# Performance work log

Measured on AMD Instinct MI355X. Metric: run time of the kernel, lower is better.

## Reference

```python
import jax, jax.numpy as jnp
import numpy as np


def setup_inputs() -> dict:
    key = jax.random.key(0)
    k1, k2, k3 = jax.random.split(key, 3)
    x = jax.random.normal(k1, (32, 256, 32, 32), dtype=jnp.float32)
    weight = jax.random.normal(k2, (256, 256, 3, 3), dtype=jnp.float32) * 0.05
    bias = jax.random.normal(k3, (256,), dtype=jnp.float32) * 0.01
    return {"x": x, "weight": weight, "bias": bias}


def _forward(x, weight, bias):
    B, cin, n, _ = x.shape
    cout, _, k, _ = weight.shape
    s = (k - 1) // 2
    nf = n // 2 + 1
    bins = n * nf

    # fft shift matrix: exp(-1j*2*pi*s*(i+j)/n), kept rfft columns
    idx = jnp.arange(n)
    shift = idx[None, :] + idx[:, None]                     # (n, n)
    shift_m = jnp.exp(-1j * 2 * jnp.pi * s * shift / n)[:, :nf]
    shift_m = shift_m.reshape(bins, 1, 1).astype(jnp.complex64)

    # xfft: (B, cin, n, nf) -> (bins, cin, B)
    xfft = jnp.fft.rfft2(x)
    xfft = jnp.transpose(xfft, (2, 3, 1, 0)).reshape(bins, cin, B)

    # Hfft: (cout, cin, n, nf) -> (bins, cout, cin), shifted + conj
    Hfft = jnp.fft.rfft2(weight, s=(n, n)).reshape(cout, cin, bins)
    Hfft = shift_m * jnp.conj(jnp.transpose(Hfft, (2, 0, 1)))

    def sq_abs(z):
        return jnp.real(z) ** 2 + jnp.imag(z) ** 2

    RowNorm = jnp.sqrt(jnp.sum(sq_abs(Hfft), axis=2))       # (bins, cout)
    ColNorm = jnp.sqrt(jnp.sum(sq_abs(Hfft), axis=1))       # (bins, cin)

    if cout >= cin:
        RowLoss = jnp.mean((RowNorm - jnp.sqrt(cin / cout)) ** 2)
        ColLoss = jnp.mean((ColNorm - 1.0) ** 2)
        HHT = jnp.einsum('npc,nqc->npq', jnp.conj(Hfft), Hfft)  # (bins, cout, cout)
        mask = jnp.triu(jnp.ones((cout, cout), bool), k=1)
        count = bins * (cout * (cout - 1) // 2)
        AngLoss = jnp.sum(sq_abs(HHT) * mask[None]) / count   # MSE(|HHT[triu]|, 0)
        L = cout * ColLoss + cin * RowLoss + AngLoss
    else:
        RowLoss = jnp.mean((RowNorm - 1.0) ** 2)
        ColLoss = jnp.mean((ColNorm - jnp.sqrt(cout / cin)) ** 2)
        HTH = jnp.einsum('ndp,ndq->npq', jnp.conj(Hfft), Hfft)  # (bins, cin, cin)
        mask = jnp.triu(jnp.ones((cin, cin), bool), k=1)
        count = bins * (cin * (cin - 1) // 2)
        AngLoss = jnp.sum(sq_abs(HTH) * mask[None]) / count
        L = cout * ColLoss + cin * RowLoss + AngLoss

    # per-bin complex matmul: (bins, cout, cin) @ (bins, cin, B) -> (bins, cout, B)
    yfft = Hfft @ xfft
    yfft = jnp.transpose(yfft.reshape(n, nf, cout, B), (3, 2, 0, 1))  # (B, cout, n, nf)
    y = jnp.fft.irfft2(yfft, s=(n, n))
    y = y + bias[None, :, None, None]
    return y, L


def reference(x, weight, bias):
    return _forward(x, weight, bias)
```

## Files before the change

kernel.cpp:

```cpp
#include <hip/hip_runtime.h>
#include <math.h>

typedef __attribute__((ext_vector_type(8)))  short  short8;
typedef __attribute__((ext_vector_type(16))) float  float16;

#define TWO_PI_OVER_32 0.19634954084936207f

static __device__ __forceinline__ unsigned short f2bf(float f) {
    unsigned int u = __float_as_uint(f);
    u = (u + 0x7FFFu + ((u >> 16) & 1u)) >> 16;
    return (unsigned short)u;
}
static __device__ __forceinline__ float bf2f(unsigned short s) {
    return __uint_as_float(((unsigned int)s) << 16);
}

static __device__ __forceinline__ void g2l16(const void* g, void* l) {
    __builtin_amdgcn_global_load_lds(
        (const __attribute__((address_space(1))) unsigned int*)g,
        (__attribute__((address_space(3))) unsigned int*)l, 16, 0, 0);
}

#define SBAR() do { __builtin_amdgcn_s_barrier(); \
                    __builtin_amdgcn_sched_barrier(0); } while (0)
#define WAITV(n) do { asm volatile("s_waitcnt vmcnt(" #n ")" ::: "memory"); \
                      __builtin_amdgcn_sched_barrier(0); } while (0)

__global__ __launch_bounds__(256) void k_prepx(const float* __restrict__ x,
                                               unsigned short* __restrict__ xb,
                                               const float* __restrict__ w,
                                               unsigned short* __restrict__ wt,
                                               unsigned short* __restrict__ Vb,
                                               float* __restrict__ Drow,
                                               float* __restrict__ Dcol) {
    __shared__ union {
        unsigned short tr[8 * 1024];
        struct { float sdata[45]; float ws2[256 * 9]; } wm;
    } sh;
    int tid = threadIdx.x;

    if (blockIdx.x < 1024) {
        int b = blockIdx.x >> 5, cig = blockIdx.x & 31;
        int r = tid >> 3, c4 = (tid & 7) * 4;
        const float4* xv = (const float4*)(x + ((size_t)(b * 256 + cig * 8)) * 1024);
        #pragma unroll
        for (int u = 0; u < 8; ++u) {
            float4 v = xv[u * 256 + r * 8 + (c4 >> 2)];
            union { unsigned short s[4]; uint2 d; } pk;
            pk.s[0] = f2bf(v.x); pk.s[1] = f2bf(v.y);
            pk.s[2] = f2bf(v.z); pk.s[3] = f2bf(v.w);
            *(uint2*)&sh.tr[u * 1024 + r * 32 + c4] = pk.d;
        }
        __syncthreads();
        uint4* dst = (uint4*)xb + ((size_t)b * 32 + cig) * 1024;
        #pragma unroll
        for (int k = 0; k < 4; ++k) {
            int g = tid * 4 + k;
            union { unsigned short u[8]; uint4 v; } pk;
            #pragma unroll
            for (int u = 0; u < 8; ++u) pk.u[u] = sh.tr[u * 1024 + g];
            dst[g] = pk.v;
        }
        return;
    }

    int blk = blockIdx.x - 1024, lane = tid & 63;
    bool colmode = blk >= 256;
    int pc = blk & 255;
    if (tid < 45) sh.wm.sdata[tid] = 0.f;

    int p = colmode ? tid : pc;
    int c = colmode ? pc : tid;
    float w9[9];
    #pragma unroll
    for (int t = 0; t < 9; ++t) w9[t] = w[(p * 256 + c) * 9 + t];
    if (!colmode) {
        #pragma unroll
        for (int t = 0; t < 9; ++t) sh.wm.ws2[tid * 9 + t] = w9[t];
    }
    __syncthreads();

    int idx = 0;
    for (int ta = 0; ta < 9; ++ta)
        for (int tb = ta; tb < 9; ++tb) {
            float v = w9[ta] * w9[tb];
            #pragma unroll
            for (int off = 32; off > 0; off >>= 1) v += __shfl_down(v, off);
            if (lane == 0) atomicAdd(&sh.wm.sdata[idx], v);
            ++idx;
        }
    __syncthreads();
    if (tid < 45) (colmode ? Dcol : Drow)[tid * 256 + pc] = sh.wm.sdata[tid];

    if (!colmode) {
        #pragma unroll
        for (int t = 0; t < 9; ++t)
            wt[t * 65536 + (c >> 3) * 2048 + p * 8 + (c & 7)] = f2bf(w9[t]);
        if (tid < 320) {
            int ta = tid >> 5, cig = tid & 31;
            union { unsigned short u[8]; uint4 v; } pk;
            #pragma unroll
            for (int u = 0; u < 8; ++u)
                pk.u[u] = (ta < 9) ? f2bf(sh.wm.ws2[(cig * 8 + u) * 9 + ta]) : (unsigned short)0;
            ((uint4*)Vb)[(p * 10 + ta) * 32 + cig] = pk.v;
        }
    }
}

__global__ __launch_bounds__(256, 3) void k_conv(const unsigned short* __restrict__ xb,
                                                 const unsigned short* __restrict__ wt,
                                                 const float* __restrict__ bias,
                                                 const unsigned short* __restrict__ Vb,
                                                 unsigned short* __restrict__ Gb,
                                                 float* __restrict__ y) {
    __shared__ unsigned short xs[640 * 8];
    __shared__ unsigned short wsm[2][1152 * 8];

    const int tid  = threadIdx.x;
    const int lane = tid & 63;
    const int half = lane >> 5;
    const int m    = lane & 31;

    if (blockIdx.x < 210) {
        int blk = blockIdx.x, I = 0;
        while (blk >= 20 - I) { blk -= 20 - I; ++I; }
        int J = I + blk;
        const int wave = tid >> 6;
        const int wm = wave >> 1, wn = wave & 1;
        const int row0 = I * 128 + wm * 64;
        const int col0 = J * 128 + wn * 64;

        float16 acc[2][2];
        #pragma unroll
        for (int i = 0; i < 2; ++i)
            #pragma unroll
            for (int j = 0; j < 2; ++j)
                #pragma unroll
                for (int r = 0; r < 16; ++r) acc[i][j][r] = 0.f;

        const short8* vb = (const short8*)Vb;
        for (int kc = 0; kc < 16; ++kc) {
            int cig = kc * 2 + half;
            short8 a0 = vb[(row0 + m) * 32 + cig];
            short8 a1 = vb[(row0 + 32 + m) * 32 + cig];
            short8 b0 = vb[(col0 + m) * 32 + cig];
            short8 b1 = vb[(col0 + 32 + m) * 32 + cig];
            acc[0][0] = __builtin_amdgcn_mfma_f32_32x32x16_bf16(a0, b0, acc[0][0], 0, 0, 0);
            acc[0][1] = __builtin_amdgcn_mfma_f32_32x32x16_bf16(a0, b1, acc[0][1], 0, 0, 0);
            acc[1][0] = __builtin_amdgcn_mfma_f32_32x32x16_bf16(a1, b0, acc[1][0], 0, 0, 0);
            acc[1][1] = __builtin_amdgcn_mfma_f32_32x32x16_bf16(a1, b1, acc[1][1], 0, 0, 0);
        }
        #pragma unroll
        for (int i = 0; i < 2; ++i)
            #pragma unroll
            for (int j = 0; j < 2; ++j)
                #pragma unroll
                for (int reg = 0; reg < 16; ++reg) {
                    int crow = (reg & 3) + 8 * (reg >> 2) + 4 * half;
                    Gb[(row0 + i * 32 + crow) * 2560 + col0 + j * 32 + m] =
                        f2bf(acc[i][j][reg]);
                }
        return;
    }

    const int wv    = tid >> 6;
    const int id    = blockIdx.x - 210;
    const int xcd   = id & 7;
    const int local = id >> 3;
    const int b     = xcd * 4 + (local >> 4);
    const int rem   = local & 15;
    const int co0   = (rem & 3) * 64;
    const int r0    = (rem >> 2) * 8;

    float16 acc[2][2];
    #pragma unroll
    for (int i = 0; i < 2; ++i)
        #pragma unroll
        for (int ns = 0; ns < 2; ++ns)
            #pragma unroll
            for (int r = 0; r < 16; ++r) acc[i][ns][r] = 0.f;

    const uint4* xbv = (const uint4*)xb;
    const uint4* wtv = (const uint4*)wt;

    const int cigl = lane >> 5;
    const int coll = lane & 31;

    auto stage_x = [&](int kc) {
        uint4* xd = (uint4*)xs;
        #pragma unroll
        for (int ch = wv; ch < 10; ch += 4) {
            int gr = (r0 + ch + 31) & 31;
            g2l16(&xbv[((b * 32 + kc * 2 + cigl) * 32 + gr) * 32 + coll],
                  &xd[ch * 64]);
        }
    };
    auto stage_w = [&](int buf, int kc) {
        uint4* wd = (uint4*)wsm[buf];
        #pragma unroll
        for (int wc = wv; wc < 18; wc += 4) {
            int t = wc >> 1, cig = wc & 1;
            g2l16(&wtv[t * 8192 + (kc * 2 + cig) * 256 + co0 + lane],
                  &wd[wc * 64]);
        }
    };

    auto compute = [&](int buf) {
        const short8* xsl = (const short8*)xs;
        const short8* wsl = (const short8*)wsm[buf];
        #pragma unroll
        for (int btv = 0; btv < 3; ++btv) {
            short8 a0[3], a1[3];
            #pragma unroll
            for (int atv = 0; atv < 3; ++atv) {
                int t = atv * 3 + btv;
                a0[atv] = wsl[(t * 2 + half) * 64 + m];
                a1[atv] = wsl[(t * 2 + half) * 64 + 32 + m];
            }
            #pragma unroll
            for (int s = 0; s < 4; ++s) {
                short8 bf = xsl[((wv * 2 + s) * 2 + half) * 32 + ((m + btv + 31) & 31)];
                #pragma unroll
                for (int atv = 0; atv < 3; ++atv) {
                    int ns = s - atv;
                    if (ns >= 0 && ns < 2) {
                        acc[0][ns] = __builtin_amdgcn_mfma_f32_32x32x16_bf16(a0[atv], bf, acc[0][ns], 0, 0, 0);
                        acc[1][ns] = __builtin_amdgcn_mfma_f32_32x32x16_bf16(a1[atv], bf, acc[1][ns], 0, 0, 0);
                    }
                }
            }
        }
    };

    stage_w(0, 0);
    stage_x(0);
    #pragma unroll 1
    for (int kc = 0; kc < 16; ++kc) {
        int buf = kc & 1;
        if (kc < 15) {
            stage_w(buf ^ 1, kc + 1);
            if (wv < 2) { WAITV(5); } else { WAITV(4); }
        } else {
            WAITV(0);
        }
        SBAR();
        __builtin_amdgcn_s_setprio(1);
        compute(buf);
        __builtin_amdgcn_s_setprio(0);
        SBAR();
        if (kc < 15) stage_x(kc + 1);
    }

    #pragma unroll
    for (int i = 0; i < 2; ++i) {
        #pragma unroll
        for (int ns = 0; ns < 2; ++ns) {
            int r = r0 + wv * 2 + ns;
            #pragma unroll
            for (int reg = 0; reg < 16; ++reg) {
                int crow = (reg & 3) + 8 * (reg >> 2) + 4 * half;
                int co = co0 + i * 32 + crow;
                y[(b * 256 + co) * 1024 + r * 32 + m] = acc[i][ns][reg] + bias[co];
            }
        }
    }
}

__global__ __launch_bounds__(256) void k_loss(const float* __restrict__ Drow,
                                              const float* __restrict__ Dcol,
                                              const unsigned short* __restrict__ Gb,
                                              float* __restrict__ rowp,
                                              float* __restrict__ colp,
                                              float* __restrict__ angp) {
    __shared__ union {
        struct { float coef[45]; float red[2]; } rc;
        struct { unsigned short gs[9 * 2560]; float red; } ang;
    } sh;
    int tid = threadIdx.x;

    if (blockIdx.x < 544) {
        int bin = blockIdx.x;
        int u = bin / 17, v = bin % 17;
        if (tid < 2) sh.rc.red[tid] = 0.f;
        if (tid < 45) {
            int idx = 0, TA = 0, TB = 0;
            for (int ta = 0; ta < 9; ++ta)
                for (int tb = ta; tb < 9; ++tb) {
                    if (idx == tid) { TA = ta; TB = tb; }
                    ++idx;
                }
            int da = TA / 3 - TB / 3;
            int db = TA % 3 - TB % 3;
            float cth = cosf(TWO_PI_OVER_32 * (float)(u * da + v * db));
            sh.rc.coef[tid] = (TA == TB) ? 1.f : 2.f * cth;
        }
        __syncthreads();

        float s1 = 0.f, s2 = 0.f;
        const float* dr = Drow + tid;
        const float* dc = Dcol + tid;
        #pragma unroll
        for (int i = 0; i < 45; ++i) {
            s1 += sh.rc.coef[i] * dr[i * 256];
            s2 += sh.rc.coef[i] * dc[i * 256];
        }
        float e1 = sqrtf(fmaxf(s1, 0.f)) - 1.f; e1 *= e1;
        float e2 = sqrtf(fmaxf(s2, 0.f)) - 1.f; e2 *= e2;
        #pragma unroll
        for (int off = 32; off > 0; off >>= 1) {
            e1 += __shfl_down(e1, off);
            e2 += __shfl_down(e2, off);
        }
        if ((tid & 63) == 0) { atomicAdd(&sh.rc.red[0], e1); atomicAdd(&sh.rc.red[1], e2); }
        __syncthreads();
        if (tid == 0) { rowp[bin] = sh.rc.red[0]; colp[bin] = sh.rc.red[1]; }
    } else {
        int p = blockIdx.x - 544;
        if (tid == 0) sh.ang.red = 0.f;
        uint4* gsv = (uint4*)sh.ang.gs;
        const uint4* gbv = (const uint4*)Gb;
        for (int i = tid; i < 2880; i += 256) {
            int rr = i / 320, cc = i - rr * 320;
            gsv[i] = gbv[(p * 10 + rr) * 320 + cc];
        }
        __syncthreads();

        int q = tid;
        float S = 0.f;
        if (q > p) {
            float g5[5][5];
            #pragma unroll
            for (int i = 0; i < 5; ++i)
                #pragma unroll
                for (int j = 0; j < 5; ++j) g5[i][j] = 0.f;
            #pragma unroll
            for (int ta = 0; ta < 9; ++ta)
                #pragma unroll
                for (int tb = 0; tb < 9; ++tb) {
                    float c = bf2f(sh.ang.gs[ta * 2560 + q * 10 + tb]);
                    g5[ta / 3 - tb / 3 + 2][ta % 3 - tb % 3 + 2] += c;
                }
            #pragma unroll
            for (int da = 0; da < 5; ++da) {
                const float* g = g5[da];
                float sq = g[0]*g[0] + g[1]*g[1] + g[2]*g[2] + g[3]*g[3] + g[4]*g[4];
                float cr = g[0]*g[2] + g[1]*g[3] + g[2]*g[4] + g[0]*g[4];
                S += 17.f * sq + 2.f * cr;
            }
            S *= 32.f;
        }
        #pragma unroll
        for (int off = 32; off > 0; off >>= 1) S += __shfl_down(S, off);
        if ((tid & 63) == 0) atomicAdd(&sh.ang.red, S);
        __syncthreads();
        if (tid == 0) angp[p] = sh.ang.red;
    }
}

__global__ __launch_bounds__(256) void k_fin(const float* __restrict__ rowp,
                                             const float* __restrict__ colp,
                                             const float* __restrict__ angp,
                                             float* __restrict__ out) {
    __shared__ float sred[3][4];
    int tid = threadIdx.x;
    float r = 0.f, c = 0.f, a = 0.f;
    for (int i = tid; i < 544; i += 256) { r += rowp[i]; c += colp[i]; }
    a = angp[tid];
    #pragma unroll
    for (int off = 32; off > 0; off >>= 1) {
        r += __shfl_down(r, off);
        c += __shfl_down(c, off);
        a += __shfl_down(a, off);
    }
    if ((tid & 63) == 0) {
        int wv = tid >> 6;
        sred[0][wv] = r; sred[1][wv] = c; sred[2][wv] = a;
    }
    __syncthreads();
    if (tid == 0) {
        float R = sred[0][0] + sred[0][1] + sred[0][2] + sred[0][3];
        float C = sred[1][0] + sred[1][1] + sred[1][2] + sred[1][3];
        float A = sred[2][0] + sred[2][1] + sred[2][2] + sred[2][3];
        out[8388608] = R / 544.f + C / 544.f + A / (544.f * 32640.f);
    }
}

extern "C" void kernel_launch(void* const* d_in, const int* in_sizes, int n_in,
                              void* d_out, int out_size, void* d_ws, size_t ws_size,
                              hipStream_t stream) {
    const float* x    = (const float*)d_in[0];
    const float* w    = (const float*)d_in[1];
    const float* bias = (const float*)d_in[2];
    float* out = (float*)d_out;

    char* ws = (char*)d_ws;
    unsigned short* wt = (unsigned short*)ws;
    unsigned short* xb = (unsigned short*)(ws + 1179648);
    unsigned short* Vb = (unsigned short*)(ws + 17956864);
    float* Drow  = (float*)(ws + 19267584);
    float* Dcol  = (float*)(ws + 19313664);
    float* rowp  = (float*)(ws + 19359744);
    float* colp  = (float*)(ws + 19361920);
    float* angp  = (float*)(ws + 19364096);
    unsigned short* Gb = (unsigned short*)(ws + 19392512);

    k_prepx <<<1536, 256, 0, stream>>>(x, xb, w, wt, Vb, Drow, Dcol);
    k_conv  <<<722, 256, 0, stream>>>(xb, wt, bias, Vb, Gb, out);
    k_loss  <<<800, 256, 0, stream>>>(Drow, Dcol, Gb, rowp, colp, angp);
    k_fin   <<<1, 256, 0, stream>>>(rowp, colp, angp, out);
}
```

Before: 153.9 us.

## Restructure conv kernel into single-wave blocks with double-buffered x and w

Measured after the change: 156.4 us. No clear change (+1.6%).

```diff
diff --git a/kernel.cpp b/kernel.cpp
--- a/kernel.cpp
+++ b/kernel.cpp
@@ -21,8 +21,6 @@
         (__attribute__((address_space(3))) unsigned int*)l, 16, 0, 0);
 }
 
-#define SBAR() do { __builtin_amdgcn_s_barrier(); \
-                    __builtin_amdgcn_sched_barrier(0); } while (0)
 #define WAITV(n) do { asm volatile("s_waitcnt vmcnt(" #n ")" ::: "memory"); \
                       __builtin_amdgcn_sched_barrier(0); } while (0)
 
@@ -107,28 +105,25 @@
     }
 }
 
-__global__ __launch_bounds__(256, 3) void k_conv(const unsigned short* __restrict__ xb,
-                                                 const unsigned short* __restrict__ wt,
-                                                 const float* __restrict__ bias,
-                                                 const unsigned short* __restrict__ Vb,
-                                                 unsigned short* __restrict__ Gb,
-                                                 float* __restrict__ y) {
-    __shared__ unsigned short xs[640 * 8];
-    __shared__ unsigned short wsm[2][1152 * 8];
-
-    const int tid  = threadIdx.x;
-    const int lane = tid & 63;
+__global__ __launch_bounds__(64, 2) void k_conv(const unsigned short* __restrict__ xb,
+                                                const unsigned short* __restrict__ wt,
+                                                const float* __restrict__ bias,
+                                                const unsigned short* __restrict__ Vb,
+                                                unsigned short* __restrict__ Gb,
+                                                float* __restrict__ y) {
+    __shared__ unsigned short xs[2][640 * 8];
+    __shared__ unsigned short wsm[2][576 * 8];
+
+    const int lane = threadIdx.x & 63;
     const int half = lane >> 5;
     const int m    = lane & 31;
 
-    if (blockIdx.x < 210) {
-        int blk = blockIdx.x, I = 0;
-        while (blk >= 20 - I) { blk -= 20 - I; ++I; }
+    if (blockIdx.x >= 1024) {
+        int blk = blockIdx.x - 1024, I = 0;
+        while (blk >= 40 - I) { blk -= 40 - I; ++I; }
         int J = I + blk;
-        const int wave = tid >> 6;
-        const int wm = wave >> 1, wn = wave & 1;
-        const int row0 = I * 128 + wm * 64;
-        const int col0 = J * 128 + wn * 64;
+        const int row0 = I * 64;
+        const int col0 = J * 64;
 
         float16 acc[2][2];
         #pragma unroll
@@ -163,22 +158,19 @@
         return;
     }
 
-    const int wv    = tid >> 6;
-    const int id    = blockIdx.x - 210;
+    const int id    = blockIdx.x;
     const int xcd   = id & 7;
     const int local = id >> 3;
-    const int b     = xcd * 4 + (local >> 4);
-    const int rem   = local & 15;
-    const int co0   = (rem & 3) * 64;
-    const int r0    = (rem >> 2) * 8;
-
-    float16 acc[2][2];
+    const int b     = xcd * 4 + (local >> 5);
+    const int rem   = local & 31;
+    const int co0   = (rem & 7) * 32;
+    const int r0    = (rem >> 3) * 8;
+
+    float16 acc[8];
     #pragma unroll
-    for (int i = 0; i < 2; ++i)
-        #pragma unroll
-        for (int ns = 0; ns < 2; ++ns)
-            #pragma unroll
-            for (int r = 0; r < 16; ++r) acc[i][ns][r] = 0.f;
+    for (int ns = 0; ns < 8; ++ns)
+        #pragma unroll
+        for (int r = 0; r < 16; ++r) acc[ns][r] = 0.f;
 
     const uint4* xbv = (const uint4*)xb;
     const uint4* wtv = (const uint4*)wt;
@@ -186,10 +178,10 @@
     const int cigl = lane >> 5;
     const int coll = lane & 31;
 
-    auto stage_x = [&](int kc) {
-        uint4* xd = (uint4*)xs;
-        #pragma unroll
-        for (int ch = wv; ch < 10; ch += 4) {
+    auto stage_x = [&](int buf, int kc) {
+        uint4* xd = (uint4*)xs[buf];
+        #pragma unroll
+        for (int ch = 0; ch < 10; ++ch) {
             int gr = (r0 + ch + 31) & 31;
             g2l16(&xbv[((b * 32 + kc * 2 + cigl) * 32 + gr) * 32 + coll],
                   &xd[ch * 64]);
@@ -198,70 +190,60 @@
     auto stage_w = [&](int buf, int kc) {
         uint4* wd = (uint4*)wsm[buf];
         #pragma unroll
-        for (int wc = wv; wc < 18; wc += 4) {
-            int t = wc >> 1, cig = wc & 1;
-            g2l16(&wtv[t * 8192 + (kc * 2 + cig) * 256 + co0 + lane],
-                  &wd[wc * 64]);
+        for (int t = 0; t < 9; ++t) {
+            g2l16(&wtv[t * 8192 + (kc * 2 + cigl) * 256 + co0 + coll],
+                  &wd[t * 64]);
         }
     };
 
     auto compute = [&](int buf) {
-        const short8* xsl = (const short8*)xs;
+        const short8* xsl = (const short8*)xs[buf];
         const short8* wsl = (const short8*)wsm[buf];
         #pragma unroll
         for (int btv = 0; btv < 3; ++btv) {
-            short8 a0[3], a1[3];
+            int gc = (m + btv + 31) & 31;
+            short8 bfr[10];
+            #pragma unroll
+            for (int sl = 0; sl < 10; ++sl)
+                bfr[sl] = xsl[(sl * 2 + half) * 32 + gc];
             #pragma unroll
             for (int atv = 0; atv < 3; ++atv) {
                 int t = atv * 3 + btv;
-                a0[atv] = wsl[(t * 2 + half) * 64 + m];
-                a1[atv] = wsl[(t * 2 + half) * 64 + 32 + m];
-            }
-            #pragma unroll
-            for (int s = 0; s < 4; ++s) {
-                short8 bf = xsl[((wv * 2 + s) * 2 + half) * 32 + ((m + btv + 31) & 31)];
-                #pragma unroll
-                for (int atv = 0; atv < 3; ++atv) {
-                    int ns = s - atv;
-                    if (ns >= 0 && ns < 2) {
-                        acc[0][ns] = __builtin_amdgcn_mfma_f32_32x32x16_bf16(a0[atv], bf, acc[0][ns], 0, 0, 0);
-                        acc[1][ns] = __builtin_amdgcn_mfma_f32_32x32x16_bf16(a1[atv], bf, acc[1][ns], 0, 0, 0);
-                    }
+                short8 a = wsl[(t * 2 + half) * 32 + m];
+                #pragma unroll
+                for (int ns = 0; ns < 8; ++ns) {
+                    acc[ns] = __builtin_amdgcn_mfma_f32_32x32x16_bf16(
+                        a, bfr[ns + atv], acc[ns], 0, 0, 0);
                 }
             }
         }
     };
 
     stage_w(0, 0);
-    stage_x(0);
+    stage_x(0, 0);
     #pragma unroll 1
     for (int kc = 0; kc < 16; ++kc) {
         int buf = kc & 1;
         if (kc < 15) {
             stage_w(buf ^ 1, kc + 1);
-            if (wv < 2) { WAITV(5); } else { WAITV(4); }
+            stage_x(buf ^ 1, kc + 1);
+            WAITV(19);
         } else {
             WAITV(0);
         }
-        SBAR();
         __builtin_amdgcn_s_setprio(1);
         compute(buf);
         __builtin_amdgcn_s_setprio(0);
-        SBAR();
-        if (kc < 15) stage_x(kc + 1);
     }
 
     #pragma unroll
-    for (int i = 0; i < 2; ++i) {
-        #pragma unroll
-        for (int ns = 0; ns < 2; ++ns) {
-            int r = r0 + wv * 2 + ns;
-            #pragma unroll
-            for (int reg = 0; reg < 16; ++reg) {
-                int crow = (reg & 3) + 8 * (reg >> 2) + 4 * half;
-                int co = co0 + i * 32 + crow;
-                y[(b * 256 + co) * 1024 + r * 32 + m] = acc[i][ns][reg] + bias[co];
-            }
+    for (int ns = 0; ns < 8; ++ns) {
+        int r = r0 + ns;
+        #pragma unroll
+        for (int reg = 0; reg < 16; ++reg) {
+            int crow = (reg & 3) + 8 * (reg >> 2) + 4 * half;
+            int co = co0 + crow;
+            y[(b * 256 + co) * 1024 + r * 32 + m] = acc[ns][reg] + bias[co];
         }
     }
 }
@@ -405,7 +387,7 @@
     unsigned short* Gb = (unsigned short*)(ws + 19392512);
 
     k_prepx <<<1536, 256, 0, stream>>>(x, xb, w, wt, Vb, Drow, Dcol);
-    k_conv  <<<722, 256, 0, stream>>>(xb, wt, bias, Vb, Gb, out);
+    k_conv  <<<1844, 64, 0, stream>>>(xb, wt, bias, Vb, Gb, out);
     k_loss  <<<800, 256, 0, stream>>>(Drow, Dcol, Gb, rowp, colp, angp);
     k_fin   <<<1, 256, 0, stream>>>(rowp, colp, angp, out);
 }
```
